# Performance work log

Measured on AMD Instinct MI355X. Metric: run time of the kernel, lower is better.

Reference implementation:

```python
import jax, jax.numpy as jnp
import numpy as np

N = 2048

def setup_inputs() -> dict:
    key = jax.random.key(0)
    kx, kq, kk, kv = jax.random.split(key, 4)
    x = jax.random.normal(kx, (N, N), dtype=jnp.float32)
    q = jax.random.normal(kq, (N, N), dtype=jnp.float32)
    k = jax.random.normal(kk, (N, N), dtype=jnp.float32)
    v = jax.random.normal(kv, (N, N), dtype=jnp.float32)
    return {"x": x, "q": q, "k": k, "v": v}

def reference(x, q, k, v):
    # qk = (x @ q) @ (x @ k)  -- note: NOT (x@k).T, faithful to torch.mm chain
    qk = jnp.matmul(jnp.matmul(x, q), jnp.matmul(x, k))  # [n, n]
    attn = jax.nn.softmax(qk, axis=-1)                   # row softmax over n
    return jnp.matmul(attn, jnp.matmul(x, v))            # [n, n]
```

## Files before the change

kernel.cpp:

```cpp
#include <hip/hip_runtime.h>
#include <stdint.h>


#define TN 2048

typedef float f32x4 __attribute__((ext_vector_type(4)));
typedef _Float16 f16;
typedef f16 f16x8 __attribute__((ext_vector_type(8)));
typedef f16 f16x4 __attribute__((ext_vector_type(4)));

#define MFMA16(a, b, c) __builtin_amdgcn_mfma_f32_16x16x32_f16(a, b, c, 0, 0, 0)
#define SBAR() asm volatile("s_barrier" ::: "memory")
#define VMCNT(n) asm volatile("s_waitcnt vmcnt(" #n ")" ::: "memory")

__device__ __forceinline__ void glds16(const f16* g, f16* l) {
    __builtin_amdgcn_global_load_lds(
        (const __attribute__((address_space(1))) unsigned int*)g,
        (__attribute__((address_space(3))) unsigned int*)l, 16, 0, 0);
}

__global__ void split2_kernel(const float* __restrict__ in,
                              f16* __restrict__ t0, f16* __restrict__ t1) {
    int i = (blockIdx.x * 256 + threadIdx.x) * 4;
    f32x4 f = *(const f32x4*)(in + i);
    f16x4 o0, o1;
#pragma unroll
    for (int e = 0; e < 4; ++e) {
        float a = f[e];
        f16 h0 = (f16)a;
        o0[e] = h0; o1[e] = (f16)(a - (float)h0);
    }
    *(f16x4*)(t0 + i) = o0; *(f16x4*)(t1 + i) = o1;
}

__global__ void split2_add_kernel(const float* __restrict__ inA,
                                  const float* __restrict__ inB,
                                  f16* __restrict__ t0, f16* __restrict__ t1) {
    int i = (blockIdx.x * 256 + threadIdx.x) * 4;
    f32x4 fa = *(const f32x4*)(inA + i);
    f32x4 fb = *(const f32x4*)(inB + i);
    f16x4 o0, o1;
#pragma unroll
    for (int e = 0; e < 4; ++e) {
        float a = fa[e] + fb[e];
        f16 h0 = (f16)a;
        o0[e] = h0; o1[e] = (f16)(a - (float)h0);
    }
    *(f16x4*)(t0 + i) = o0; *(f16x4*)(t1 + i) = o1;
}

__global__ void split2t_kernel(const float* __restrict__ in,
                               f16* __restrict__ t0, f16* __restrict__ t1) {
    __shared__ f16 s0[64][68], s1[64][68];
    int bc = blockIdx.x * 64, br = blockIdx.y * 64;
    int tx = threadIdx.x & 15, ty = threadIdx.x >> 4;
#pragma unroll
    for (int rr = 0; rr < 64; rr += 16) {
        int r = rr + ty;
        f32x4 f = *(const f32x4*)(in + (size_t)(br + r) * TN + bc + tx * 4);
#pragma unroll
        for (int e = 0; e < 4; ++e) {
            float a = f[e];
            f16 h0 = (f16)a;
            s0[tx * 4 + e][r] = h0; s1[tx * 4 + e][r] = (f16)(a - (float)h0);
        }
    }
    __syncthreads();
#pragma unroll
    for (int rr = 0; rr < 64; rr += 16) {
        int c = rr + ty;
        f16x4 o0, o1;
#pragma unroll
        for (int e = 0; e < 4; ++e) { o0[e] = s0[c][tx*4+e]; o1[e] = s1[c][tx*4+e]; }
        size_t off = (size_t)(bc + c) * TN + br + tx * 4;
        *(f16x4*)(t0 + off) = o0; *(f16x4*)(t1 + off) = o1;
    }
}

__global__ void split2t_add_kernel(const float* __restrict__ inA,
                                   const float* __restrict__ inB,
                                   f16* __restrict__ t0, f16* __restrict__ t1) {
    __shared__ f16 s0[64][68], s1[64][68];
    int bc = blockIdx.x * 64, br = blockIdx.y * 64;
    int tx = threadIdx.x & 15, ty = threadIdx.x >> 4;
#pragma unroll
    for (int rr = 0; rr < 64; rr += 16) {
        int r = rr + ty;
        size_t off = (size_t)(br + r) * TN + bc + tx * 4;
        f32x4 fa = *(const f32x4*)(inA + off);
        f32x4 fb = *(const f32x4*)(inB + off);
#pragma unroll
        for (int e = 0; e < 4; ++e) {
            float a = fa[e] + fb[e];
            f16 h0 = (f16)a;
            s0[tx * 4 + e][r] = h0; s1[tx * 4 + e][r] = (f16)(a - (float)h0);
        }
    }
    __syncthreads();
#pragma unroll
    for (int rr = 0; rr < 64; rr += 16) {
        int c = rr + ty;
        f16x4 o0, o1;
#pragma unroll
        for (int e = 0; e < 4; ++e) { o0[e] = s0[c][tx*4+e]; o1[e] = s1[c][tx*4+e]; }
        size_t off = (size_t)(bc + c) * TN + br + tx * 4;
        *(f16x4*)(t0 + off) = o0; *(f16x4*)(t1 + off) = o1;
    }
}

__global__ void cast1t_kernel(const float* __restrict__ in, f16* __restrict__ t0) {
    __shared__ f16 s0[64][68];
    int bc = blockIdx.x * 64, br = blockIdx.y * 64;
    int tx = threadIdx.x & 15, ty = threadIdx.x >> 4;
#pragma unroll
    for (int rr = 0; rr < 64; rr += 16) {
        int r = rr + ty;
        f32x4 f = *(const f32x4*)(in + (size_t)(br + r) * TN + bc + tx * 4);
#pragma unroll
        for (int e = 0; e < 4; ++e) s0[tx * 4 + e][r] = (f16)f[e];
    }
    __syncthreads();
#pragma unroll
    for (int rr = 0; rr < 64; rr += 16) {
        int c = rr + ty;
        f16x4 o0;
#pragma unroll
        for (int e = 0; e < 4; ++e) o0[e] = s0[c][tx*4+e];
        *(f16x4*)(t0 + (size_t)(bc + c) * TN + br + tx * 4) = o0;
    }
}

__global__ void cast1t_add_kernel(const float* __restrict__ inA,
                                  const float* __restrict__ inB,
                                  f16* __restrict__ t0) {
    __shared__ f16 s0[64][68];
    int bc = blockIdx.x * 64, br = blockIdx.y * 64;
    int tx = threadIdx.x & 15, ty = threadIdx.x >> 4;
#pragma unroll
    for (int rr = 0; rr < 64; rr += 16) {
        int r = rr + ty;
        size_t off = (size_t)(br + r) * TN + bc + tx * 4;
        f32x4 fa = *(const f32x4*)(inA + off);
        f32x4 fb = *(const f32x4*)(inB + off);
#pragma unroll
        for (int e = 0; e < 4; ++e) s0[tx * 4 + e][r] = (f16)(fa[e] + fb[e]);
    }
    __syncthreads();
#pragma unroll
    for (int rr = 0; rr < 64; rr += 16) {
        int c = rr + ty;
        f16x4 o0;
#pragma unroll
        for (int e = 0; e < 4; ++e) o0[e] = s0[c][tx*4+e];
        *(f16x4*)(t0 + (size_t)(bc + c) * TN + br + tx * 4) = o0;
    }
}

__global__ void final_add_kernel(const float* __restrict__ inA,
                                 const float* __restrict__ inB,
                                 float* __restrict__ out) {
    int i = (blockIdx.x * 256 + threadIdx.x) * 4;
    f32x4 fa = *(const f32x4*)(inA + i);
    f32x4 fb = *(const f32x4*)(inB + i);
    f32x4 o;
#pragma unroll
    for (int e = 0; e < 4; ++e) o[e] = fa[e] + fb[e];
    *(f32x4*)(out + i) = o;
}

__global__ __launch_bounds__(512, 2) void gemm3_f16(
    const f16* __restrict__ a0p, const f16* __restrict__ a1p,
    const f16* __restrict__ b0p, const f16* __restrict__ b1p,
    float* __restrict__ C0, float* __restrict__ C1) {
    __shared__ f16 lds[3][48 * 512];
    const int tid = threadIdx.x;
    const int wave = tid >> 6, lane = tid & 63;
    const int wrow = wave >> 2, wcol = wave & 3;
    const int quad = lane >> 4, l16 = lane & 15;
    const int bm = blockIdx.y * 128, bn = blockIdx.x * 256;
    const int kbase = blockIdx.z * 1024;
    float* __restrict__ C = blockIdx.z ? C1 : C0;

    const int ws = wave * 6;
    const f16* sp[6];
#pragma unroll
    for (int t = 0; t < 6; ++t) {
        int s = ws + t;
        const f16* base; int gr;
        if (s < 8)       { base = a0p; gr = bm + s * 16 + l16; }
        else if (s < 16) { base = a1p; gr = bm + (s - 8) * 16 + l16; }
        else if (s < 32) { base = b0p; gr = bn + (s - 16) * 16 + l16; }
        else             { base = b1p; gr = bn + (s - 32) * 16 + l16; }
        sp[t] = base + (size_t)gr * TN + kbase + quad * 8;
    }
    const int rof = lane * 8;
    const int sa0 = wrow * 4, sa1 = 8 + wrow * 4;
    const int sb0 = 16 + wcol * 4, sb1 = 32 + wcol * 4;

    f32x4 acc[4][4];
#pragma unroll
    for (int i = 0; i < 4; ++i)
#pragma unroll
        for (int j = 0; j < 4; ++j) acc[i][j] = (f32x4){0.f, 0.f, 0.f, 0.f};

#pragma unroll
    for (int t = 0; t < 6; ++t) { glds16(sp[t], &lds[0][(ws + t) * 512]); sp[t] += 32; }
#pragma unroll
    for (int t = 0; t < 6; ++t) { glds16(sp[t], &lds[1][(ws + t) * 512]); sp[t] += 32; }
    f16* cur = &lds[0][0]; f16* nxt = &lds[1][0]; f16* pre = &lds[2][0];
    VMCNT(6); SBAR();

    f16x8 a0f[4], a1f[4], b0f[4], b1f[4];
#pragma unroll
    for (int i = 0; i < 4; ++i) a0f[i] = *(const f16x8*)(cur + (sa0 + i) * 512 + rof);
#pragma unroll
    for (int j = 0; j < 4; ++j) b0f[j] = *(const f16x8*)(cur + (sb0 + j) * 512 + rof);

    for (int step = 0; step < 32; ++step) {
#pragma unroll
        for (int j = 0; j < 4; ++j) b1f[j] = *(const f16x8*)(cur + (sb1 + j) * 512 + rof);
        if (step < 30) {
#pragma unroll
            for (int t = 0; t < 3; ++t) { glds16(sp[t], pre + (ws + t) * 512); sp[t] += 32; }
        }
        SBAR();
        __builtin_amdgcn_s_setprio(1);
#pragma unroll
        for (int i = 0; i < 4; ++i)
#pragma unroll
            for (int j = 0; j < 4; ++j) acc[i][j] = MFMA16(a0f[i], b0f[j], acc[i][j]);
        __builtin_amdgcn_s_setprio(0);
#pragma unroll
        for (int i = 0; i < 4; ++i) a1f[i] = *(const f16x8*)(cur + (sa1 + i) * 512 + rof);
        if (step < 30) {
#pragma unroll
            for (int t = 3; t < 6; ++t) { glds16(sp[t], pre + (ws + t) * 512); sp[t] += 32; }
        }
        SBAR();
        __builtin_amdgcn_s_setprio(1);
#pragma unroll
        for (int i = 0; i < 4; ++i)
#pragma unroll
            for (int j = 0; j < 4; ++j) acc[i][j] = MFMA16(a0f[i], b1f[j], acc[i][j]);
        __builtin_amdgcn_s_setprio(0);
        __builtin_amdgcn_s_setprio(1);
#pragma unroll
        for (int i = 0; i < 4; ++i)
#pragma unroll
            for (int j = 0; j < 4; ++j) acc[i][j] = MFMA16(a1f[i], b0f[j], acc[i][j]);
        __builtin_amdgcn_s_setprio(0);
        if (step < 31) {
            if (step < 30) { VMCNT(6); } else { VMCNT(0); }
            SBAR();
#pragma unroll
            for (int i = 0; i < 4; ++i) a0f[i] = *(const f16x8*)(nxt + (sa0 + i) * 512 + rof);
#pragma unroll
            for (int j = 0; j < 4; ++j) b0f[j] = *(const f16x8*)(nxt + (sb0 + j) * 512 + rof);
        }
        f16* tmp = cur; cur = nxt; nxt = pre; pre = tmp;
    }
#pragma unroll
    for (int i = 0; i < 4; ++i)
#pragma unroll
        for (int j = 0; j < 4; ++j) {
            int row = bm + wrow * 64 + i * 16 + quad * 4;
            int col = bn + wcol * 64 + j * 16 + l16;
            float* p = C + (size_t)row * TN + col;
#pragma unroll
            for (int r = 0; r < 4; ++r) p[(size_t)r * TN] = acc[i][j][r];
        }
}

__global__ __launch_bounds__(256, 2) void gemm1_f16(
    const f16* __restrict__ A, const f16* __restrict__ Bt,
    float* __restrict__ C0, float* __restrict__ C1) {
    __shared__ f16 lds[3][16 * 512];
    const int tid = threadIdx.x;
    const int wave = tid >> 6, lane = tid & 63;
    const int wr = (wave >> 1) * 64, wc = (wave & 1) * 64;
    const int quad = lane >> 4, l16 = lane & 15;
    const int bm = blockIdx.y * 128, bn = blockIdx.x * 128;
    const int kbase = blockIdx.z * 1024;
    float* __restrict__ C = blockIdx.z ? C1 : C0;

    const int ws = wave * 4;
    const f16* sp[4];
#pragma unroll
    for (int t = 0; t < 4; ++t) {
        int s = ws + t;
        const f16* base; int gr;
        if (s < 8) { base = A;  gr = bm + s * 16 + l16; }
        else       { base = Bt; gr = bn + (s - 8) * 16 + l16; }
        sp[t] = base + (size_t)gr * TN + kbase + quad * 8;
    }
    const int rof = lane * 8;
    const int sa = (wr >> 4), sb = 8 + (wc >> 4);

    f32x4 acc[4][4];
#pragma unroll
    for (int i = 0; i < 4; ++i)
#pragma unroll
        for (int j = 0; j < 4; ++j) acc[i][j] = (f32x4){0.f, 0.f, 0.f, 0.f};

#pragma unroll
    for (int t = 0; t < 4; ++t) { glds16(sp[t], &lds[0][(ws + t) * 512]); sp[t] += 32; }
#pragma unroll
    for (int t = 0; t < 4; ++t) { glds16(sp[t], &lds[1][(ws + t) * 512]); sp[t] += 32; }
    f16* cur = &lds[0][0]; f16* nxt = &lds[1][0]; f16* pre = &lds[2][0];
    VMCNT(4); SBAR();

    f16x8 af[4], bf[4];
#pragma unroll
    for (int i = 0; i < 4; ++i) af[i] = *(const f16x8*)(cur + (sa + i) * 512 + rof);
#pragma unroll
    for (int j = 0; j < 4; ++j) bf[j] = *(const f16x8*)(cur + (sb + j) * 512 + rof);

    for (int step = 0; step < 32; ++step) {
        if (step < 30) {
#pragma unroll
            for (int t = 0; t < 4; ++t) { glds16(sp[t], pre + (ws + t) * 512); sp[t] += 32; }
        }
        SBAR();
        __builtin_amdgcn_s_setprio(1);
#pragma unroll
        for (int i = 0; i < 4; ++i)
#pragma unroll
            for (int j = 0; j < 4; ++j) acc[i][j] = MFMA16(af[i], bf[j], acc[i][j]);
        __builtin_amdgcn_s_setprio(0);
        if (step < 31) {
            if (step < 30) { VMCNT(4); } else { VMCNT(0); }
            SBAR();
#pragma unroll
            for (int i = 0; i < 4; ++i) af[i] = *(const f16x8*)(nxt + (sa + i) * 512 + rof);
#pragma unroll
            for (int j = 0; j < 4; ++j) bf[j] = *(const f16x8*)(nxt + (sb + j) * 512 + rof);
        }
        f16* tmp = cur; cur = nxt; nxt = pre; pre = tmp;
    }
#pragma unroll
    for (int i = 0; i < 4; ++i)
#pragma unroll
        for (int j = 0; j < 4; ++j) {
            int row = bm + wr + i * 16 + quad * 4;
            int col = bn + wc + j * 16 + l16;
            float* p = C + (size_t)row * TN + col;
#pragma unroll
            for (int r = 0; r < 4; ++r) p[(size_t)r * TN] = acc[i][j][r];
        }
}

__global__ void softmax_add_kernel(const float* __restrict__ S0,
                                   const float* __restrict__ S1,
                                   f16* __restrict__ P) {
    __shared__ float red[256];
    const int row = blockIdx.x, tid = threadIdx.x;
    const size_t base = (size_t)row * TN + tid * 8;
    f32x4 a0 = *(const f32x4*)(S0 + base);
    f32x4 a1 = *(const f32x4*)(S0 + base + 4);
    f32x4 b0 = *(const f32x4*)(S1 + base);
    f32x4 b1 = *(const f32x4*)(S1 + base + 4);
    float vals[8];
#pragma unroll
    for (int e = 0; e < 4; ++e) { vals[e] = a0[e] + b0[e]; vals[4 + e] = a1[e] + b1[e]; }
    float m = vals[0];
#pragma unroll
    for (int e = 1; e < 8; ++e) m = fmaxf(m, vals[e]);
    red[tid] = m; __syncthreads();
    for (int st = 128; st > 0; st >>= 1) { if (tid < st) red[tid] = fmaxf(red[tid], red[tid + st]); __syncthreads(); }
    m = red[0]; __syncthreads();
    float sum = 0.f;
#pragma unroll
    for (int e = 0; e < 8; ++e) { vals[e] = expf(vals[e] - m); sum += vals[e]; }
    red[tid] = sum; __syncthreads();
    for (int st = 128; st > 0; st >>= 1) { if (tid < st) red[tid] += red[tid + st]; __syncthreads(); }
    float inv = 1.f / red[0];
    f16x8 o;
#pragma unroll
    for (int e = 0; e < 8; ++e) o[e] = (f16)(vals[e] * inv);
    *(f16x8*)(P + base) = o;
}

extern "C" void kernel_launch(void* const* d_in, const int* in_sizes, int n_in,
                              void* d_out, int out_size, void* d_ws, size_t ws_size,
                              hipStream_t stream) {
    const float* x = (const float*)d_in[0];
    const float* q = (const float*)d_in[1];
    const float* k = (const float*)d_in[2];
    const float* v = (const float*)d_in[3];
    float* out = (float*)d_out;
    const size_t M = (size_t)TN * TN;

    float* W1 = (float*)d_ws;
    float* W2 = W1 + M;
    f16* pl = (f16*)(W2 + M);
    f16 *x0 = pl,         *x1 = pl + M;
    f16 *q0 = pl + 2 * M, *q1 = pl + 3 * M;
    f16 *k0 = pl + 4 * M, *k1 = pl + 5 * M;
    f16 *v0 = pl + 6 * M;
    f16 *a0 = q0, *a1 = q1;
    f16 *b0 = k0, *b1 = k1;
    f16 *p0 = x1, *c0 = x0;

    dim3 bs(256), bs3(512);
    dim3 gelem(TN * TN / 4 / 256);
    dim3 gt(TN / 64, TN / 64);
    dim3 gg3(TN / 256, TN / 128, 2);
    dim3 gg1(TN / 128, TN / 128, 2);

    hipLaunchKernelGGL(split2_kernel,  gelem, bs, 0, stream, x, x0, x1);
    hipLaunchKernelGGL(cast1t_kernel,  gt,    bs, 0, stream, v, v0);
    hipLaunchKernelGGL(split2t_kernel, gt,    bs, 0, stream, q, q0, q1);
    hipLaunchKernelGGL(gemm3_f16, gg3, bs3, 0, stream, x0, x1, q0, q1, W1, W2);
    hipLaunchKernelGGL(split2_add_kernel, gelem, bs, 0, stream, W1, W2, a0, a1);
    hipLaunchKernelGGL(split2t_kernel, gt, bs, 0, stream, k, k0, k1);
    hipLaunchKernelGGL(gemm3_f16, gg3, bs3, 0, stream, x0, x1, k0, k1, W1, W2);
    hipLaunchKernelGGL(split2t_add_kernel, gt, bs, 0, stream, W1, W2, b0, b1);
    hipLaunchKernelGGL(gemm3_f16, gg3, bs3, 0, stream, a0, a1, b0, b1, W1, W2);
    hipLaunchKernelGGL(softmax_add_kernel, dim3(TN), bs, 0, stream, W1, W2, p0);
    hipLaunchKernelGGL(gemm1_f16, gg1, bs, 0, stream, x0, v0, W1, W2);
    hipLaunchKernelGGL(cast1t_add_kernel, gt, bs, 0, stream, W1, W2, c0);
    hipLaunchKernelGGL(gemm1_f16, gg1, bs, 0, stream, p0, c0, W1, W2);
    hipLaunchKernelGGL(final_add_kernel, gelem, bs, 0, stream, W1, W2, out);
}
```

Before: 390.8 us.

## Replace split-K gemm1 with full-K kernel writing fused epilogues directly

The single-precision-split GEMM1 now runs over the full K range with a 64x128 tile and 64-wide K steps, replacing the split-K z=2 scheme. Its epilogue either writes a transposed fp16 result directly (for x@v) or the final fp32 output, which removes the cast1t_add and final_add kernels and the fp32 partial round-trips. Extra barriers are added to gemm3 between MFMA phases. Dropping split-K halves the grid parallelism per GEMM and lengthens each block's K loop, and the transposed fp16 stores may be poorly coalesced.

```diff
diff --git a/kernel.cpp b/kernel.cpp
--- a/kernel.cpp
+++ b/kernel.cpp
@@ -128,44 +128,6 @@
         for (int e = 0; e < 4; ++e) o0[e] = s0[c][tx*4+e];
         *(f16x4*)(t0 + (size_t)(bc + c) * TN + br + tx * 4) = o0;
     }
-}
-
-__global__ void cast1t_add_kernel(const float* __restrict__ inA,
-                                  const float* __restrict__ inB,
-                                  f16* __restrict__ t0) {
-    __shared__ f16 s0[64][68];
-    int bc = blockIdx.x * 64, br = blockIdx.y * 64;
-    int tx = threadIdx.x & 15, ty = threadIdx.x >> 4;
-#pragma unroll
-    for (int rr = 0; rr < 64; rr += 16) {
-        int r = rr + ty;
-        size_t off = (size_t)(br + r) * TN + bc + tx * 4;
-        f32x4 fa = *(const f32x4*)(inA + off);
-        f32x4 fb = *(const f32x4*)(inB + off);
-#pragma unroll
-        for (int e = 0; e < 4; ++e) s0[tx * 4 + e][r] = (f16)(fa[e] + fb[e]);
-    }
-    __syncthreads();
-#pragma unroll
-    for (int rr = 0; rr < 64; rr += 16) {
-        int c = rr + ty;
-        f16x4 o0;
-#pragma unroll
-        for (int e = 0; e < 4; ++e) o0[e] = s0[c][tx*4+e];
-        *(f16x4*)(t0 + (size_t)(bc + c) * TN + br + tx * 4) = o0;
-    }
-}
-
-__global__ void final_add_kernel(const float* __restrict__ inA,
-                                 const float* __restrict__ inB,
-                                 float* __restrict__ out) {
-    int i = (blockIdx.x * 256 + threadIdx.x) * 4;
-    f32x4 fa = *(const f32x4*)(inA + i);
-    f32x4 fb = *(const f32x4*)(inB + i);
-    f32x4 o;
-#pragma unroll
-    for (int e = 0; e < 4; ++e) o[e] = fa[e] + fb[e];
-    *(f32x4*)(out + i) = o;
 }
 
 __global__ __launch_bounds__(512, 2) void gemm3_f16(
@@ -230,6 +192,7 @@
 #pragma unroll
             for (int j = 0; j < 4; ++j) acc[i][j] = MFMA16(a0f[i], b0f[j], acc[i][j]);
         __builtin_amdgcn_s_setprio(0);
+        SBAR();
 #pragma unroll
         for (int i = 0; i < 4; ++i) a1f[i] = *(const f16x8*)(cur + (sa1 + i) * 512 + rof);
         if (step < 30) {
@@ -243,6 +206,7 @@
 #pragma unroll
             for (int j = 0; j < 4; ++j) acc[i][j] = MFMA16(a0f[i], b1f[j], acc[i][j]);
         __builtin_amdgcn_s_setprio(0);
+        SBAR();
         __builtin_amdgcn_s_setprio(1);
 #pragma unroll
         for (int i = 0; i < 4; ++i)
@@ -271,82 +235,118 @@
         }
 }
 
-__global__ __launch_bounds__(256, 2) void gemm1_f16(
+__global__ __launch_bounds__(256, 2) void gemm1_fused(
     const f16* __restrict__ A, const f16* __restrict__ Bt,
-    float* __restrict__ C0, float* __restrict__ C1) {
-    __shared__ f16 lds[3][16 * 512];
+    float* __restrict__ outF, f16* __restrict__ outH, int mode) {
+    __shared__ f16 lds[3][24 * 512];
     const int tid = threadIdx.x;
     const int wave = tid >> 6, lane = tid & 63;
-    const int wr = (wave >> 1) * 64, wc = (wave & 1) * 64;
+    const int wr = (wave >> 1) * 32, wc = (wave & 1) * 64;
     const int quad = lane >> 4, l16 = lane & 15;
-    const int bm = blockIdx.y * 128, bn = blockIdx.x * 128;
-    const int kbase = blockIdx.z * 1024;
-    float* __restrict__ C = blockIdx.z ? C1 : C0;
-
-    const int ws = wave * 4;
-    const f16* sp[4];
-#pragma unroll
-    for (int t = 0; t < 4; ++t) {
-        int s = ws + t;
+    const int bm = blockIdx.y * 64, bn = blockIdx.x * 128;
+
+    const f16* sp[6];
+#pragma unroll
+    for (int t = 0; t < 6; ++t) {
+        int s = wave * 3 + (t >> 1);
+        int kh = t & 1;
         const f16* base; int gr;
-        if (s < 8) { base = A;  gr = bm + s * 16 + l16; }
-        else       { base = Bt; gr = bn + (s - 8) * 16 + l16; }
-        sp[t] = base + (size_t)gr * TN + kbase + quad * 8;
+        if (s < 4) { base = A;  gr = bm + s * 16 + l16; }
+        else       { base = Bt; gr = bn + (s - 4) * 16 + l16; }
+        sp[t] = base + (size_t)gr * TN + kh * 32 + quad * 8;
     }
     const int rof = lane * 8;
-    const int sa = (wr >> 4), sb = 8 + (wc >> 4);
-
-    f32x4 acc[4][4];
-#pragma unroll
-    for (int i = 0; i < 4; ++i)
+    const int sa = (wr >> 4) , sb = 4 + (wc >> 4) ;
+
+    f32x4 acc[2][4];
+#pragma unroll
+    for (int i = 0; i < 2; ++i)
 #pragma unroll
         for (int j = 0; j < 4; ++j) acc[i][j] = (f32x4){0.f, 0.f, 0.f, 0.f};
 
 #pragma unroll
-    for (int t = 0; t < 4; ++t) { glds16(sp[t], &lds[0][(ws + t) * 512]); sp[t] += 32; }
-#pragma unroll
-    for (int t = 0; t < 4; ++t) { glds16(sp[t], &lds[1][(ws + t) * 512]); sp[t] += 32; }
+    for (int t = 0; t < 6; ++t) {
+        int ds = ((wave * 3 + (t >> 1)) * 2 + (t & 1)) * 512;
+        glds16(sp[t], &lds[0][ds]); sp[t] += 64;
+    }
+#pragma unroll
+    for (int t = 0; t < 6; ++t) {
+        int ds = ((wave * 3 + (t >> 1)) * 2 + (t & 1)) * 512;
+        glds16(sp[t], &lds[1][ds]); sp[t] += 64;
+    }
     f16* cur = &lds[0][0]; f16* nxt = &lds[1][0]; f16* pre = &lds[2][0];
-    VMCNT(4); SBAR();
-
-    f16x8 af[4], bf[4];
-#pragma unroll
-    for (int i = 0; i < 4; ++i) af[i] = *(const f16x8*)(cur + (sa + i) * 512 + rof);
-#pragma unroll
-    for (int j = 0; j < 4; ++j) bf[j] = *(const f16x8*)(cur + (sb + j) * 512 + rof);
+    VMCNT(6); SBAR();
+
+    f16x8 af[2][2], bf[4][2];
+#pragma unroll
+    for (int i = 0; i < 2; ++i)
+#pragma unroll
+        for (int kh = 0; kh < 2; ++kh)
+            af[i][kh] = *(const f16x8*)(cur + ((sa + i) * 2 + kh) * 512 + rof);
+#pragma unroll
+    for (int j = 0; j < 4; ++j)
+#pragma unroll
+        for (int kh = 0; kh < 2; ++kh)
+            bf[j][kh] = *(const f16x8*)(cur + ((sb + j) * 2 + kh) * 512 + rof);
 
     for (int step = 0; step < 32; ++step) {
         if (step < 30) {
 #pragma unroll
-            for (int t = 0; t < 4; ++t) { glds16(sp[t], pre + (ws + t) * 512); sp[t] += 32; }
+            for (int t = 0; t < 6; ++t) {
+                int ds = ((wave * 3 + (t >> 1)) * 2 + (t & 1)) * 512;
+                glds16(sp[t], pre + ds); sp[t] += 64;
+            }
         }
         SBAR();
         __builtin_amdgcn_s_setprio(1);
 #pragma unroll
-        for (int i = 0; i < 4; ++i)
-#pragma unroll
-            for (int j = 0; j < 4; ++j) acc[i][j] = MFMA16(af[i], bf[j], acc[i][j]);
+        for (int kh = 0; kh < 2; ++kh)
+#pragma unroll
+            for (int i = 0; i < 2; ++i)
+#pragma unroll
+                for (int j = 0; j < 4; ++j)
+                    acc[i][j] = MFMA16(af[i][kh], bf[j][kh], acc[i][j]);
         __builtin_amdgcn_s_setprio(0);
         if (step < 31) {
-            if (step < 30) { VMCNT(4); } else { VMCNT(0); }
+            if (step < 30) { VMCNT(6); } else { VMCNT(0); }
             SBAR();
 #pragma unroll
-            for (int i = 0; i < 4; ++i) af[i] = *(const f16x8*)(nxt + (sa + i) * 512 + rof);
-#pragma unroll
-            for (int j = 0; j < 4; ++j) bf[j] = *(const f16x8*)(nxt + (sb + j) * 512 + rof);
+            for (int i = 0; i < 2; ++i)
+#pragma unroll
+                for (int kh = 0; kh < 2; ++kh)
+                    af[i][kh] = *(const f16x8*)(nxt + ((sa + i) * 2 + kh) * 512 + rof);
+#pragma unroll
+            for (int j = 0; j < 4; ++j)
+#pragma unroll
+                for (int kh = 0; kh < 2; ++kh)
+                    bf[j][kh] = *(const f16x8*)(nxt + ((sb + j) * 2 + kh) * 512 + rof);
         }
         f16* tmp = cur; cur = nxt; nxt = pre; pre = tmp;
     }
-#pragma unroll
-    for (int i = 0; i < 4; ++i)
-#pragma unroll
-        for (int j = 0; j < 4; ++j) {
-            int row = bm + wr + i * 16 + quad * 4;
-            int col = bn + wc + j * 16 + l16;
-            float* p = C + (size_t)row * TN + col;
-#pragma unroll
-            for (int r = 0; r < 4; ++r) p[(size_t)r * TN] = acc[i][j][r];
-        }
+    if (mode == 0) {
+#pragma unroll
+        for (int i = 0; i < 2; ++i)
+#pragma unroll
+            for (int j = 0; j < 4; ++j) {
+                int row = bm + wr + i * 16 + quad * 4;
+                int col = bn + wc + j * 16 + l16;
+                float* p = outF + (size_t)row * TN + col;
+#pragma unroll
+                for (int r = 0; r < 4; ++r) p[(size_t)r * TN] = acc[i][j][r];
+            }
+    } else {
+#pragma unroll
+        for (int i = 0; i < 2; ++i)
+#pragma unroll
+            for (int j = 0; j < 4; ++j) {
+                int row = bm + wr + i * 16 + quad * 4;
+                int col = bn + wc + j * 16 + l16;
+                f16x4 h;
+#pragma unroll
+                for (int r = 0; r < 4; ++r) h[r] = (f16)acc[i][j][r];
+                *(f16x4*)(outH + (size_t)col * TN + row) = h;
+            }
+    }
 }
 
 __global__ void softmax_add_kernel(const float* __restrict__ S0,
@@ -399,13 +399,14 @@
     f16 *v0 = pl + 6 * M;
     f16 *a0 = q0, *a1 = q1;
     f16 *b0 = k0, *b1 = k1;
-    f16 *p0 = x1, *c0 = x0;
+    f16 *p0 = x1;
+    f16 *c0 = q0;
 
     dim3 bs(256), bs3(512);
     dim3 gelem(TN * TN / 4 / 256);
     dim3 gt(TN / 64, TN / 64);
     dim3 gg3(TN / 256, TN / 128, 2);
-    dim3 gg1(TN / 128, TN / 128, 2);
+    dim3 gg1(TN / 128, TN / 64);
 
     hipLaunchKernelGGL(split2_kernel,  gelem, bs, 0, stream, x, x0, x1);
     hipLaunchKernelGGL(cast1t_kernel,  gt,    bs, 0, stream, v, v0);
@@ -417,8 +418,6 @@
     hipLaunchKernelGGL(split2t_add_kernel, gt, bs, 0, stream, W1, W2, b0, b1);
     hipLaunchKernelGGL(gemm3_f16, gg3, bs3, 0, stream, a0, a1, b0, b1, W1, W2);
     hipLaunchKernelGGL(softmax_add_kernel, dim3(TN), bs, 0, stream, W1, W2, p0);
-    hipLaunchKernelGGL(gemm1_f16, gg1, bs, 0, stream, x0, v0, W1, W2);
-    hipLaunchKernelGGL(cast1t_add_kernel, gt, bs, 0, stream, W1, W2, c0);
-    hipLaunchKernelGGL(gemm1_f16, gg1, bs, 0, stream, p0, c0, W1, W2);
-    hipLaunchKernelGGL(final_add_kernel, gelem, bs, 0, stream, W1, W2, out);
-}
+    hipLaunchKernelGGL(gemm1_fused, gg1, bs, 0, stream, x0, v0, (float*)nullptr, c0, 1);
+    hipLaunchKernelGGL(gemm1_fused, gg1, bs, 0, stream, p0, c0, out, (f16*)nullptr, 0);
+}
```

Measured after the change: 399.0 us. +2.1%, slower.

## Shrink split-precision GEMM tile to 128x128 with double buffering

Applied to the files above, without the earlier changes.

Changes the three-term split-f16 GEMM from 512-thread blocks with 128x256 output tiles and a triple-buffered LDS prefetch to 256-thread blocks with 128x128 tiles and a two-buffer scheme. Each step now waits for all loads (vmcnt 0) and adds extra barriers to guard the buffer being refilled. This uses less LDS per block and launches twice as many blocks, which may improve occupancy and balance across CUs. In exchange it loses reuse of the A operand across a wider N tile and exposes more load latency because there is less prefetch depth.

```diff
diff --git a/kernel.cpp b/kernel.cpp
--- a/kernel.cpp
+++ b/kernel.cpp
@@ -168,34 +168,34 @@
     *(f32x4*)(out + i) = o;
 }
 
-__global__ __launch_bounds__(512, 2) void gemm3_f16(
+__global__ __launch_bounds__(256, 2) void gemm3_f16(
     const f16* __restrict__ a0p, const f16* __restrict__ a1p,
     const f16* __restrict__ b0p, const f16* __restrict__ b1p,
     float* __restrict__ C0, float* __restrict__ C1) {
-    __shared__ f16 lds[3][48 * 512];
+    __shared__ f16 lds[2][32 * 512];
     const int tid = threadIdx.x;
     const int wave = tid >> 6, lane = tid & 63;
-    const int wrow = wave >> 2, wcol = wave & 3;
+    const int wr = (wave >> 1) * 64, wc = (wave & 1) * 64;
     const int quad = lane >> 4, l16 = lane & 15;
-    const int bm = blockIdx.y * 128, bn = blockIdx.x * 256;
+    const int bm = blockIdx.y * 128, bn = blockIdx.x * 128;
     const int kbase = blockIdx.z * 1024;
     float* __restrict__ C = blockIdx.z ? C1 : C0;
 
-    const int ws = wave * 6;
-    const f16* sp[6];
-#pragma unroll
-    for (int t = 0; t < 6; ++t) {
+    const int ws = wave * 8;
+    const f16* sp[8];
+#pragma unroll
+    for (int t = 0; t < 8; ++t) {
         int s = ws + t;
         const f16* base; int gr;
         if (s < 8)       { base = a0p; gr = bm + s * 16 + l16; }
         else if (s < 16) { base = a1p; gr = bm + (s - 8) * 16 + l16; }
-        else if (s < 32) { base = b0p; gr = bn + (s - 16) * 16 + l16; }
-        else             { base = b1p; gr = bn + (s - 32) * 16 + l16; }
+        else if (s < 24) { base = b0p; gr = bn + (s - 16) * 16 + l16; }
+        else             { base = b1p; gr = bn + (s - 24) * 16 + l16; }
         sp[t] = base + (size_t)gr * TN + kbase + quad * 8;
     }
     const int rof = lane * 8;
-    const int sa0 = wrow * 4, sa1 = 8 + wrow * 4;
-    const int sb0 = 16 + wcol * 4, sb1 = 32 + wcol * 4;
+    const int sa0 = (wave >> 1) * 4, sa1 = 8 + (wave >> 1) * 4;
+    const int sb0 = 16 + (wave & 1) * 4, sb1 = 24 + (wave & 1) * 4;
 
     f32x4 acc[4][4];
 #pragma unroll
@@ -204,11 +204,9 @@
         for (int j = 0; j < 4; ++j) acc[i][j] = (f32x4){0.f, 0.f, 0.f, 0.f};
 
 #pragma unroll
-    for (int t = 0; t < 6; ++t) { glds16(sp[t], &lds[0][(ws + t) * 512]); sp[t] += 32; }
-#pragma unroll
-    for (int t = 0; t < 6; ++t) { glds16(sp[t], &lds[1][(ws + t) * 512]); sp[t] += 32; }
-    f16* cur = &lds[0][0]; f16* nxt = &lds[1][0]; f16* pre = &lds[2][0];
-    VMCNT(6); SBAR();
+    for (int t = 0; t < 8; ++t) { glds16(sp[t], &lds[0][(ws + t) * 512]); sp[t] += 32; }
+    f16* cur = &lds[0][0]; f16* nxt = &lds[1][0];
+    VMCNT(0); SBAR();
 
     f16x8 a0f[4], a1f[4], b0f[4], b1f[4];
 #pragma unroll
@@ -219,9 +217,9 @@
     for (int step = 0; step < 32; ++step) {
 #pragma unroll
         for (int j = 0; j < 4; ++j) b1f[j] = *(const f16x8*)(cur + (sb1 + j) * 512 + rof);
-        if (step < 30) {
-#pragma unroll
-            for (int t = 0; t < 3; ++t) { glds16(sp[t], pre + (ws + t) * 512); sp[t] += 32; }
+        if (step < 31) {
+#pragma unroll
+            for (int t = 0; t < 4; ++t) { glds16(sp[t], nxt + (ws + t) * 512); sp[t] += 32; }
         }
         SBAR();
         __builtin_amdgcn_s_setprio(1);
@@ -230,11 +228,12 @@
 #pragma unroll
             for (int j = 0; j < 4; ++j) acc[i][j] = MFMA16(a0f[i], b0f[j], acc[i][j]);
         __builtin_amdgcn_s_setprio(0);
+        SBAR();
 #pragma unroll
         for (int i = 0; i < 4; ++i) a1f[i] = *(const f16x8*)(cur + (sa1 + i) * 512 + rof);
-        if (step < 30) {
-#pragma unroll
-            for (int t = 3; t < 6; ++t) { glds16(sp[t], pre + (ws + t) * 512); sp[t] += 32; }
+        if (step < 31) {
+#pragma unroll
+            for (int t = 4; t < 8; ++t) { glds16(sp[t], nxt + (ws + t) * 512); sp[t] += 32; }
         }
         SBAR();
         __builtin_amdgcn_s_setprio(1);
@@ -243,6 +242,7 @@
 #pragma unroll
             for (int j = 0; j < 4; ++j) acc[i][j] = MFMA16(a0f[i], b1f[j], acc[i][j]);
         __builtin_amdgcn_s_setprio(0);
+        SBAR();
         __builtin_amdgcn_s_setprio(1);
 #pragma unroll
         for (int i = 0; i < 4; ++i)
@@ -250,21 +250,21 @@
             for (int j = 0; j < 4; ++j) acc[i][j] = MFMA16(a1f[i], b0f[j], acc[i][j]);
         __builtin_amdgcn_s_setprio(0);
         if (step < 31) {
-            if (step < 30) { VMCNT(6); } else { VMCNT(0); }
+            VMCNT(0);
             SBAR();
 #pragma unroll
             for (int i = 0; i < 4; ++i) a0f[i] = *(const f16x8*)(nxt + (sa0 + i) * 512 + rof);
 #pragma unroll
             for (int j = 0; j < 4; ++j) b0f[j] = *(const f16x8*)(nxt + (sb0 + j) * 512 + rof);
         }
-        f16* tmp = cur; cur = nxt; nxt = pre; pre = tmp;
+        f16* tmp = cur; cur = nxt; nxt = tmp;
     }
 #pragma unroll
     for (int i = 0; i < 4; ++i)
 #pragma unroll
         for (int j = 0; j < 4; ++j) {
-            int row = bm + wrow * 64 + i * 16 + quad * 4;
-            int col = bn + wcol * 64 + j * 16 + l16;
+            int row = bm + wr + i * 16 + quad * 4;
+            int col = bn + wc + j * 16 + l16;
             float* p = C + (size_t)row * TN + col;
 #pragma unroll
             for (int r = 0; r < 4; ++r) p[(size_t)r * TN] = acc[i][j][r];
@@ -401,24 +401,23 @@
     f16 *b0 = k0, *b1 = k1;
     f16 *p0 = x1, *c0 = x0;
 
-    dim3 bs(256), bs3(512);
+    dim3 bs(256);
     dim3 gelem(TN * TN / 4 / 256);
     dim3 gt(TN / 64, TN / 64);
-    dim3 gg3(TN / 256, TN / 128, 2);
-    dim3 gg1(TN / 128, TN / 128, 2);
+    dim3 gg(TN / 128, TN / 128, 2);
 
     hipLaunchKernelGGL(split2_kernel,  gelem, bs, 0, stream, x, x0, x1);
     hipLaunchKernelGGL(cast1t_kernel,  gt,    bs, 0, stream, v, v0);
     hipLaunchKernelGGL(split2t_kernel, gt,    bs, 0, stream, q, q0, q1);
-    hipLaunchKernelGGL(gemm3_f16, gg3, bs3, 0, stream, x0, x1, q0, q1, W1, W2);
+    hipLaunchKernelGGL(gemm3_f16, gg, bs, 0, stream, x0, x1, q0, q1, W1, W2);
     hipLaunchKernelGGL(split2_add_kernel, gelem, bs, 0, stream, W1, W2, a0, a1);
     hipLaunchKernelGGL(split2t_kernel, gt, bs, 0, stream, k, k0, k1);
-    hipLaunchKernelGGL(gemm3_f16, gg3, bs3, 0, stream, x0, x1, k0, k1, W1, W2);
+    hipLaunchKernelGGL(gemm3_f16, gg, bs, 0, stream, x0, x1, k0, k1, W1, W2);
     hipLaunchKernelGGL(split2t_add_kernel, gt, bs, 0, stream, W1, W2, b0, b1);
-    hipLaunchKernelGGL(gemm3_f16, gg3, bs3, 0, stream, a0, a1, b0, b1, W1, W2);
+    hipLaunchKernelGGL(gemm3_f16, gg, bs, 0, stream, a0, a1, b0, b1, W1, W2);
     hipLaunchKernelGGL(softmax_add_kernel, dim3(TN), bs, 0, stream, W1, W2, p0);
-    hipLaunchKernelGGL(gemm1_f16, gg1, bs, 0, stream, x0, v0, W1, W2);
+    hipLaunchKernelGGL(gemm1_f16, gg, bs, 0, stream, x0, v0, W1, W2);
     hipLaunchKernelGGL(cast1t_add_kernel, gt, bs, 0, stream, W1, W2, c0);
-    hipLaunchKernelGGL(gemm1_f16, gg1, bs, 0, stream, p0, c0, W1, W2);
+    hipLaunchKernelGGL(gemm1_f16, gg, bs, 0, stream, p0, c0, W1, W2);
     hipLaunchKernelGGL(final_add_kernel, gelem, bs, 0, stream, W1, W2, out);
 }
```

New measurement: 424.2 us. 8.6% more time.

## Fuse x@q and x@k into one split-f16 GEMM launch with 256x256 tiles

Applied to the files above, without the earlier changes.

Adds a gemmqk kernel that computes x@q and x@k in a single launch, with larger 256x256 tiles and double-buffered LDS. This doubles the grid to fill more CUs and lets each block reuse its x tile across more columns. The extra fp32 partial outputs go to spare workspace and the output buffer, and the fused path is used only when the workspace is large enough. Extra barriers are also added to the existing gemm3 kernel, which may add synchronization stalls there.

```diff
diff --git a/kernel.cpp b/kernel.cpp
--- a/kernel.cpp
+++ b/kernel.cpp
@@ -166,6 +166,113 @@
 #pragma unroll
     for (int e = 0; e < 4; ++e) o[e] = fa[e] + fb[e];
     *(f32x4*)(out + i) = o;
+}
+
+__global__ __launch_bounds__(512, 2) void gemmqk_f16(
+    const f16* __restrict__ a0p, const f16* __restrict__ a1p,
+    const f16* __restrict__ q0p, const f16* __restrict__ q1p,
+    const f16* __restrict__ k0p, const f16* __restrict__ k1p,
+    float* __restrict__ Wq0, float* __restrict__ Wq1,
+    float* __restrict__ Wk0, float* __restrict__ Wk1) {
+    __shared__ f16 lds[2][64 * 512];
+    const int tid = threadIdx.x;
+    const int wave = tid >> 6, lane = tid & 63;
+    const int wrow = wave >> 1, wcol = wave & 1;
+    const int quad = lane >> 4, l16 = lane & 15;
+    const int bm = blockIdx.y * 256;
+    const int bnf = blockIdx.x * 256;
+    const int bsel = bnf >= TN;
+    const int bc = bnf & (TN - 1);
+    const int kbase = blockIdx.z * 1024;
+    const f16* __restrict__ b0p = bsel ? k0p : q0p;
+    const f16* __restrict__ b1p = bsel ? k1p : q1p;
+    float* __restrict__ C = bsel ? (blockIdx.z ? Wk1 : Wk0)
+                                 : (blockIdx.z ? Wq1 : Wq0);
+
+    const int ws = wave * 8;
+    const f16* sp[8];
+#pragma unroll
+    for (int t = 0; t < 8; ++t) {
+        int s = ws + t;
+        const f16* base; int gr;
+        if (s < 16)      { base = a0p; gr = bm + s * 16 + l16; }
+        else if (s < 32) { base = a1p; gr = bm + (s - 16) * 16 + l16; }
+        else if (s < 48) { base = b0p; gr = bc + (s - 32) * 16 + l16; }
+        else             { base = b1p; gr = bc + (s - 48) * 16 + l16; }
+        sp[t] = base + (size_t)gr * TN + kbase + quad * 8;
+    }
+    const int rof = lane * 8;
+    const int sa0 = wrow * 4,      sa1 = 16 + wrow * 4;
+    const int sb0 = 32 + wcol * 8, sb1 = 48 + wcol * 8;
+
+    f32x4 acc[4][8];
+#pragma unroll
+    for (int i = 0; i < 4; ++i)
+#pragma unroll
+        for (int j = 0; j < 8; ++j) acc[i][j] = (f32x4){0.f, 0.f, 0.f, 0.f};
+
+#pragma unroll
+    for (int t = 0; t < 8; ++t) { glds16(sp[t], &lds[0][(ws + t) * 512]); sp[t] += 32; }
+    f16* cur = &lds[0][0]; f16* nxt = &lds[1][0];
+    VMCNT(0); SBAR();
+
+    f16x8 a0f[4], a1f[4], b0f[8], b1f[8];
+#pragma unroll
+    for (int i = 0; i < 4; ++i) a0f[i] = *(const f16x8*)(cur + (sa0 + i) * 512 + rof);
+#pragma unroll
+    for (int j = 0; j < 8; ++j) b0f[j] = *(const f16x8*)(cur + (sb0 + j) * 512 + rof);
+
+    for (int step = 0; step < 32; ++step) {
+#pragma unroll
+        for (int i = 0; i < 4; ++i) a1f[i] = *(const f16x8*)(cur + (sa1 + i) * 512 + rof);
+        if (step < 31) {
+#pragma unroll
+            for (int t = 0; t < 8; ++t) { glds16(sp[t], nxt + (ws + t) * 512); sp[t] += 32; }
+        }
+        SBAR();
+        __builtin_amdgcn_s_setprio(1);
+#pragma unroll
+        for (int i = 0; i < 4; ++i)
+#pragma unroll
+            for (int j = 0; j < 8; ++j) acc[i][j] = MFMA16(a0f[i], b0f[j], acc[i][j]);
+        __builtin_amdgcn_s_setprio(0);
+        SBAR();
+#pragma unroll
+        for (int j = 0; j < 8; ++j) b1f[j] = *(const f16x8*)(cur + (sb1 + j) * 512 + rof);
+        SBAR();
+        __builtin_amdgcn_s_setprio(1);
+#pragma unroll
+        for (int i = 0; i < 4; ++i)
+#pragma unroll
+            for (int j = 0; j < 8; ++j) acc[i][j] = MFMA16(a1f[i], b0f[j], acc[i][j]);
+        __builtin_amdgcn_s_setprio(0);
+        SBAR();
+        __builtin_amdgcn_s_setprio(1);
+#pragma unroll
+        for (int i = 0; i < 4; ++i)
+#pragma unroll
+            for (int j = 0; j < 8; ++j) acc[i][j] = MFMA16(a0f[i], b1f[j], acc[i][j]);
+        __builtin_amdgcn_s_setprio(0);
+        if (step < 31) {
+            VMCNT(0);
+            SBAR();
+#pragma unroll
+            for (int i = 0; i < 4; ++i) a0f[i] = *(const f16x8*)(nxt + (sa0 + i) * 512 + rof);
+#pragma unroll
+            for (int j = 0; j < 8; ++j) b0f[j] = *(const f16x8*)(nxt + (sb0 + j) * 512 + rof);
+        }
+        f16* tmp = cur; cur = nxt; nxt = tmp;
+    }
+#pragma unroll
+    for (int i = 0; i < 4; ++i)
+#pragma unroll
+        for (int j = 0; j < 8; ++j) {
+            int row = bm + wrow * 64 + i * 16 + quad * 4;
+            int col = bc + wcol * 128 + j * 16 + l16;
+            float* p = C + (size_t)row * TN + col;
+#pragma unroll
+            for (int r = 0; r < 4; ++r) p[(size_t)r * TN] = acc[i][j][r];
+        }
 }
 
 __global__ __launch_bounds__(512, 2) void gemm3_f16(
@@ -230,6 +337,7 @@
 #pragma unroll
             for (int j = 0; j < 4; ++j) acc[i][j] = MFMA16(a0f[i], b0f[j], acc[i][j]);
         __builtin_amdgcn_s_setprio(0);
+        SBAR();
 #pragma unroll
         for (int i = 0; i < 4; ++i) a1f[i] = *(const f16x8*)(cur + (sa1 + i) * 512 + rof);
         if (step < 30) {
@@ -243,6 +351,7 @@
 #pragma unroll
             for (int j = 0; j < 4; ++j) acc[i][j] = MFMA16(a0f[i], b1f[j], acc[i][j]);
         __builtin_amdgcn_s_setprio(0);
+        SBAR();
         __builtin_amdgcn_s_setprio(1);
 #pragma unroll
         for (int i = 0; i < 4; ++i)
@@ -400,21 +509,35 @@
     f16 *a0 = q0, *a1 = q1;
     f16 *b0 = k0, *b1 = k1;
     f16 *p0 = x1, *c0 = x0;
+    float* W4 = (float*)(pl + 7 * M);
+    float* W3 = out;
 
     dim3 bs(256), bs3(512);
     dim3 gelem(TN * TN / 4 / 256);
     dim3 gt(TN / 64, TN / 64);
     dim3 gg3(TN / 256, TN / 128, 2);
+    dim3 ggqk(2 * TN / 256, TN / 256, 2);
     dim3 gg1(TN / 128, TN / 128, 2);
+
+    const size_t need = (size_t)(3 * 4 + 7 * 2) * M;
 
     hipLaunchKernelGGL(split2_kernel,  gelem, bs, 0, stream, x, x0, x1);
     hipLaunchKernelGGL(cast1t_kernel,  gt,    bs, 0, stream, v, v0);
     hipLaunchKernelGGL(split2t_kernel, gt,    bs, 0, stream, q, q0, q1);
-    hipLaunchKernelGGL(gemm3_f16, gg3, bs3, 0, stream, x0, x1, q0, q1, W1, W2);
-    hipLaunchKernelGGL(split2_add_kernel, gelem, bs, 0, stream, W1, W2, a0, a1);
-    hipLaunchKernelGGL(split2t_kernel, gt, bs, 0, stream, k, k0, k1);
-    hipLaunchKernelGGL(gemm3_f16, gg3, bs3, 0, stream, x0, x1, k0, k1, W1, W2);
-    hipLaunchKernelGGL(split2t_add_kernel, gt, bs, 0, stream, W1, W2, b0, b1);
+
+    if (ws_size >= need) {
+        hipLaunchKernelGGL(split2t_kernel, gt, bs, 0, stream, k, k0, k1);
+        hipLaunchKernelGGL(gemmqk_f16, ggqk, bs3, 0, stream,
+                           x0, x1, q0, q1, k0, k1, W1, W2, W3, W4);
+        hipLaunchKernelGGL(split2_add_kernel,  gelem, bs, 0, stream, W1, W2, a0, a1);
+        hipLaunchKernelGGL(split2t_add_kernel, gt,    bs, 0, stream, W3, W4, b0, b1);
+    } else {
+        hipLaunchKernelGGL(gemm3_f16, gg3, bs3, 0, stream, x0, x1, q0, q1, W1, W2);
+        hipLaunchKernelGGL(split2_add_kernel, gelem, bs, 0, stream, W1, W2, a0, a1);
+        hipLaunchKernelGGL(split2t_kernel, gt, bs, 0, stream, k, k0, k1);
+        hipLaunchKernelGGL(gemm3_f16, gg3, bs3, 0, stream, x0, x1, k0, k1, W1, W2);
+        hipLaunchKernelGGL(split2t_add_kernel, gt, bs, 0, stream, W1, W2, b0, b1);
+    }
     hipLaunchKernelGGL(gemm3_f16, gg3, bs3, 0, stream, a0, a1, b0, b1, W1, W2);
     hipLaunchKernelGGL(softmax_add_kernel, dim3(TN), bs, 0, stream, W1, W2, p0);
     hipLaunchKernelGGL(gemm1_f16, gg1, bs, 0, stream, x0, v0, W1, W2);
```

Result: faster. 383.0 us (-2.0%).
